# Optimization experiments

Hardware: AMD Instinct MI355X
Metric: run time of the kernel (lower is better)

The kernel has to match this reference:

```python
import jax, jax.numpy as jnp
import numpy as np

D_MODEL = 1024
D_FF = 4096
N_EXPERTS = 8
TOP_K = 2
AUX_COEF = 0.01
ZLOSS_COEF = 0.001
EPS = 1e-9


def setup_inputs() -> dict:
    key = jax.random.key(0)
    k0, k1, k2, k3 = jax.random.split(key, 4)
    x = jax.random.normal(k0, (4, 2048, D_MODEL), dtype=jnp.float32)
    router_w = jax.random.normal(k1, (N_EXPERTS, D_MODEL), dtype=jnp.float32) * 0.02
    w1 = jax.random.normal(k2, (N_EXPERTS, D_FF, D_MODEL), dtype=jnp.float32) * 0.02
    b1 = jnp.zeros((N_EXPERTS, D_FF), dtype=jnp.float32)
    w2 = jax.random.normal(k3, (N_EXPERTS, D_MODEL, D_FF), dtype=jnp.float32) * 0.02
    b2 = jnp.zeros((N_EXPERTS, D_MODEL), dtype=jnp.float32)
    return {"x": x, "router_w": router_w, "w1": w1, "b1": b1, "w2": w2, "b2": b2}


def reference(x, router_w, w1, b1, w2, b2):
    B, T, D = x.shape
    N = B * T
    xf = x.reshape(N, D)

    # Router: logits [N, E], softmax probs, top-k selection + renormalized weights
    logits = jnp.einsum('nd,ed->ne', xf, router_w)
    probs = jax.nn.softmax(logits, axis=-1)
    topk_vals, topk_idx = jax.lax.top_k(probs, TOP_K)  # [N, K]
    topk_w = topk_vals / (topk_vals.sum(axis=-1, keepdims=True) + EPS)

    # Dense combine weights [N, E] (top-k indices are unique per row)
    combine = jnp.zeros((N, N_EXPERTS), dtype=xf.dtype)
    combine = combine.at[jnp.arange(N)[:, None], topk_idx].add(topk_w)

    # Per-expert MLP (fixed small loop over experts), weighted combine.
    # drop_tokens=False => no capacity truncation; masked-dense == gather/scatter math.
    y = jnp.zeros_like(xf)
    for e in range(N_EXPERTS):
        h = jax.nn.gelu(jnp.einsum('nd,fd->nf', xf, w1[e]) + b1[e], approximate=False)
        out_e = jnp.einsum('nf,df->nd', h, w2[e]) + b2[e]
        y = y + out_e * combine[:, e:e + 1]

    # Aux losses / stats
    importance = probs.sum(axis=0)                                   # [E]
    expert_load = jnp.zeros((N_EXPERTS,), jnp.float32).at[topk_idx.reshape(-1)].add(1.0)
    imp_n = importance / (importance.sum() + EPS)
    load_n = expert_load / (expert_load.sum() + EPS)
    balance_loss = N_EXPERTS * jnp.sum(imp_n * load_n)
    z_loss = jnp.mean(jax.nn.logsumexp(logits, axis=-1) ** 2)
    aux_loss = AUX_COEF * balance_loss + ZLOSS_COEF * z_loss

    return y.reshape(B, T, D), aux_loss, expert_load, importance
```

## Files before the change

### kernel.cpp

```cpp
#include <hip/hip_runtime.h>
#include <math.h>

#define NTOK 8192
#define DMODEL 1024
#define DFF 4096
#define NEXP 8
#define TILE 256
#define MAXTILES 72
#define MAXROWS (MAXTILES * TILE)
#define MOE_EPS 1e-9f
#define REG 8192

typedef unsigned short u16;
typedef __bf16 bf16x8 __attribute__((ext_vector_type(8)));
typedef float f32x4 __attribute__((ext_vector_type(4)));

struct Ctrl {
    int counts[NEXP];
    int fill[NEXP];
    int padded_off[NEXP];
    int n_tiles;
    int tile_expert[MAXTILES];
    int tile_base[MAXTILES];
    int tile_valid[MAXTILES];
    float imp[NEXP];
    float zacc;
};

__device__ __forceinline__ u16 f2bf(float f) {
    unsigned u = __float_as_uint(f);
    unsigned r = u + 0x7fffu + ((u >> 16) & 1u);
    return (u16)(r >> 16);
}

__device__ __forceinline__ void load16(const void* g, void* l) {
    __builtin_amdgcn_global_load_lds((__attribute__((address_space(1))) void*)g,
                                     (__attribute__((address_space(3))) void*)l,
                                     16, 0, 0);
}

__device__ __forceinline__ float gelu_fast(float h) {
    float u = h * (1.5957691216f + 0.0713548162f * h * h);
    return h / (1.f + __expf(-u));
}

__global__ __launch_bounds__(256) void k_convert(const float* __restrict__ src,
                                                 u16* __restrict__ dst, int n4) {
    int i = blockIdx.x * 256 + threadIdx.x;
    int stride = gridDim.x * 256;
    for (; i < n4; i += stride) {
        float4 v = ((const float4*)src)[i];
        ushort4 o;
        o.x = f2bf(v.x); o.y = f2bf(v.y); o.z = f2bf(v.z); o.w = f2bf(v.w);
        ((ushort4*)dst)[i] = o;
    }
}

__global__ __launch_bounds__(256) void k_router(const float* __restrict__ x,
                                                const float* __restrict__ rw,
                                                u16* __restrict__ xb,
                                                int* __restrict__ top_idx,
                                                float* __restrict__ top_w,
                                                Ctrl* __restrict__ ctrl) {
    __shared__ float srw[NEXP * DMODEL];
    __shared__ float simp[NEXP];
    __shared__ float szl;
    int tid = threadIdx.x;
    for (int i = tid; i < NEXP * DMODEL / 4; i += 256)
        ((float4*)srw)[i] = ((const float4*)rw)[i];
    if (tid < NEXP) simp[tid] = 0.f;
    if (tid == 0) szl = 0.f;
    __syncthreads();

    int lane = tid & 63;
    int n = blockIdx.x * 4 + (tid >> 6);
    float p[NEXP];
#pragma unroll
    for (int e = 0; e < NEXP; ++e) p[e] = 0.f;
    const float4* xr = (const float4*)(x + (size_t)n * DMODEL);
    u16 xs[16];
#pragma unroll
    for (int j = 0; j < 4; ++j) {
        float4 xv = xr[lane * 4 + j];
        int d = (lane * 4 + j) * 4;
        xs[j * 4 + 0] = f2bf(xv.x);
        xs[j * 4 + 1] = f2bf(xv.y);
        xs[j * 4 + 2] = f2bf(xv.z);
        xs[j * 4 + 3] = f2bf(xv.w);
#pragma unroll
        for (int e = 0; e < NEXP; ++e) {
            const float* r = srw + e * DMODEL + d;
            p[e] += xv.x * r[0] + xv.y * r[1] + xv.z * r[2] + xv.w * r[3];
        }
    }
    {
        uint4* dst = (uint4*)(xb + (size_t)n * DMODEL + lane * 16);
        dst[0] = ((const uint4*)xs)[0];
        dst[1] = ((const uint4*)xs)[1];
    }
#pragma unroll
    for (int e = 0; e < NEXP; ++e) {
#pragma unroll
        for (int off = 32; off > 0; off >>= 1) p[e] += __shfl_xor(p[e], off);
    }
    if (lane == 0) {
        float m = p[0];
#pragma unroll
        for (int e = 1; e < NEXP; ++e) m = fmaxf(m, p[e]);
        float pr[NEXP];
        float s = 0.f;
#pragma unroll
        for (int e = 0; e < NEXP; ++e) { pr[e] = expf(p[e] - m); s += pr[e]; }
        float inv = 1.f / s;
#pragma unroll
        for (int e = 0; e < NEXP; ++e) pr[e] *= inv;
        float lse = m + logf(s);
        int i0 = 0; float v0 = pr[0];
#pragma unroll
        for (int e = 1; e < NEXP; ++e) if (pr[e] > v0) { v0 = pr[e]; i0 = e; }
        int i1 = -1; float v1 = -1.f;
#pragma unroll
        for (int e = 0; e < NEXP; ++e) if (e != i0 && pr[e] > v1) { v1 = pr[e]; i1 = e; }
        float den = v0 + v1 + MOE_EPS;
        top_idx[n * 2] = i0;
        top_idx[n * 2 + 1] = i1;
        top_w[n * 2] = v0 / den;
        top_w[n * 2 + 1] = v1 / den;
#pragma unroll
        for (int e = 0; e < NEXP; ++e) atomicAdd(&simp[e], pr[e]);
        atomicAdd(&szl, lse * lse);
    }
    __syncthreads();
    if (tid < NEXP) atomicAdd(&ctrl->imp[tid], simp[tid]);
    if (tid == 255) atomicAdd(&ctrl->zacc, szl);
}

__global__ __launch_bounds__(256) void k_build(const int* __restrict__ top_idx,
                                               Ctrl* __restrict__ ctrl,
                                               int* __restrict__ tok_idx,
                                               float* __restrict__ tok_w) {
    __shared__ int cnt[NEXP];
    __shared__ int off[NEXP];
    __shared__ int tiles[NEXP];
    int tid = threadIdx.x;
    if (tid < NEXP) cnt[tid] = 0;
    __syncthreads();
    for (int i = tid; i < NTOK * 2; i += 256) atomicAdd(&cnt[top_idx[i]], 1);
    __syncthreads();
    if (tid == 0) {
        int o = 0, t = 0;
        for (int e = 0; e < NEXP; ++e) {
            int c = cnt[e];
            int te = (c + TILE - 1) / TILE;
            ctrl->counts[e] = c;
            ctrl->padded_off[e] = o;
            off[e] = o;
            tiles[e] = te;
            for (int i = 0; i < te; ++i) {
                ctrl->tile_expert[t] = e;
                ctrl->tile_base[t] = o + i * TILE;
                int v = c - i * TILE;
                ctrl->tile_valid[t] = v > TILE ? TILE : v;
                ++t;
            }
            o += te * TILE;
        }
        ctrl->n_tiles = t;
    }
    __syncthreads();
    for (int e = 0; e < NEXP; ++e) {
        int start = off[e] + cnt[e];
        int end = off[e] + tiles[e] * TILE;
        for (int i = start + tid; i < end; i += 256) {
            tok_idx[i] = 0;
            tok_w[i] = 0.f;
        }
    }
}

__global__ __launch_bounds__(256) void k_fill(const int* __restrict__ top_idx,
                                              const float* __restrict__ top_w,
                                              Ctrl* __restrict__ ctrl,
                                              int* __restrict__ tok_idx,
                                              float* __restrict__ tok_w) {
    int n = blockIdx.x * 256 + threadIdx.x;
    if (n >= NTOK) return;
#pragma unroll
    for (int k = 0; k < 2; ++k) {
        int e = top_idx[n * 2 + k];
        int pos = atomicAdd(&ctrl->fill[e], 1);
        int slot = ctrl->padded_off[e] + pos;
        tok_idx[slot] = n;
        tok_w[slot] = top_w[n * 2 + k];
    }
}


#define KLOOP_PHASES(STA, STB, NK)                                                    \
    STA(0, 0, 0); STB(0, 0, 0); STA(0, 0, 1); STB(0, 0, 1); STA(1, 1, 0); STB(1, 1, 0); \
    asm volatile("s_waitcnt vmcnt(8)" ::: "memory");                                  \
    __builtin_amdgcn_s_barrier();                                                     \
    for (int kt = 0; kt < (NK); ++kt) {                                               \
        int p = kt & 1;                                                               \
        const u16* A0 = sA + (p * 2 + 0) * REG;                                       \
        const u16* A1 = sA + (p * 2 + 1) * REG;                                       \
        const u16* B0 = sB + (p * 2 + 0) * REG;                                       \
        const u16* B1 = sB + (p * 2 + 1) * REG;                                       \
        bf16x8 a[4], b[4];                                                            \
                                                    \
        _Pragma("unroll") for (int m = 0; m < 4; ++m) a[m] = *(const bf16x8*)(A0 + aoff[m]); \
        _Pragma("unroll") for (int n = 0; n < 4; ++n) b[n] = *(const bf16x8*)(B0 + boff[n]); \
        if (kt + 1 < (NK)) { STA(p ^ 1, kt + 1, 1); }                                 \
        asm volatile("s_waitcnt lgkmcnt(0)" ::: "memory");                            \
        __builtin_amdgcn_sched_barrier(0);                                            \
        __builtin_amdgcn_s_setprio(1);                                                \
        _Pragma("unroll") for (int m = 0; m < 4; ++m)                                 \
            _Pragma("unroll") for (int n = 0; n < 4; ++n)                             \
                acc[m][n] = __builtin_amdgcn_mfma_f32_16x16x32_bf16(a[m], b[n], acc[m][n], 0, 0, 0); \
        __builtin_amdgcn_s_setprio(0);                                                \
        __builtin_amdgcn_sched_barrier(0);                                            \
        __builtin_amdgcn_s_barrier();                                                 \
                                                    \
        _Pragma("unroll") for (int m = 0; m < 4; ++m) a[m] = *(const bf16x8*)(A0 + aoff[m + 4]); \
        if (kt + 1 < (NK)) { STB(p ^ 1, kt + 1, 1); }                                 \
        asm volatile("s_waitcnt lgkmcnt(0)" ::: "memory");                            \
        __builtin_amdgcn_sched_barrier(0);                                            \
        __builtin_amdgcn_s_setprio(1);                                                \
        _Pragma("unroll") for (int m = 0; m < 4; ++m)                                 \
            _Pragma("unroll") for (int n = 0; n < 4; ++n)                             \
                acc[m + 4][n] = __builtin_amdgcn_mfma_f32_16x16x32_bf16(a[m], b[n], acc[m + 4][n], 0, 0, 0); \
        __builtin_amdgcn_s_setprio(0);                                                \
        __builtin_amdgcn_sched_barrier(0);                                            \
        if (kt <= (NK) - 2) asm volatile("s_waitcnt vmcnt(8)" ::: "memory");          \
        else                asm volatile("s_waitcnt vmcnt(0)" ::: "memory");          \
        __builtin_amdgcn_s_barrier();                                                 \
                                                    \
        _Pragma("unroll") for (int m = 0; m < 4; ++m) a[m] = *(const bf16x8*)(A1 + aoff[m]); \
        _Pragma("unroll") for (int n = 0; n < 4; ++n) b[n] = *(const bf16x8*)(B1 + boff[n]); \
        if (kt + 2 < (NK)) { STA(p, kt + 2, 0); }                                     \
        asm volatile("s_waitcnt lgkmcnt(0)" ::: "memory");                            \
        __builtin_amdgcn_sched_barrier(0);                                            \
        __builtin_amdgcn_s_setprio(1);                                                \
        _Pragma("unroll") for (int m = 0; m < 4; ++m)                                 \
            _Pragma("unroll") for (int n = 0; n < 4; ++n)                             \
                acc[m][n] = __builtin_amdgcn_mfma_f32_16x16x32_bf16(a[m], b[n], acc[m][n], 0, 0, 0); \
        __builtin_amdgcn_s_setprio(0);                                                \
        __builtin_amdgcn_sched_barrier(0);                                            \
        __builtin_amdgcn_s_barrier();                                                 \
                                                    \
        _Pragma("unroll") for (int m = 0; m < 4; ++m) a[m] = *(const bf16x8*)(A1 + aoff[m + 4]); \
        if (kt + 2 < (NK)) { STB(p, kt + 2, 0); }                                     \
        asm volatile("s_waitcnt lgkmcnt(0)" ::: "memory");                            \
        __builtin_amdgcn_sched_barrier(0);                                            \
        __builtin_amdgcn_s_setprio(1);                                                \
        _Pragma("unroll") for (int m = 0; m < 4; ++m)                                 \
            _Pragma("unroll") for (int n = 0; n < 4; ++n)                             \
                acc[m + 4][n] = __builtin_amdgcn_mfma_f32_16x16x32_bf16(a[m], b[n], acc[m + 4][n], 0, 0, 0); \
        __builtin_amdgcn_s_setprio(0);                                                \
        __builtin_amdgcn_sched_barrier(0);                                            \
        if (kt < (NK) - 1) {                                                          \
            if (kt <= (NK) - 3) asm volatile("s_waitcnt vmcnt(8)" ::: "memory");      \
            else                asm volatile("s_waitcnt vmcnt(0)" ::: "memory");      \
            __builtin_amdgcn_s_barrier();                                             \
        }                                                                             \
    }

__global__ __launch_bounds__(512, 2) void k_gemm1(const u16* __restrict__ xb,
                                                  const u16* __restrict__ w1b,
                                                  const float* __restrict__ b1,
                                                  const int* __restrict__ tok_idx,
                                                  const Ctrl* __restrict__ ctrl,
                                                  u16* __restrict__ H) {
    int t = blockIdx.x;
    if (t >= ctrl->n_tiles) return;
    int e = ctrl->tile_expert[t];
    int rbase = ctrl->tile_base[t];
    int n0 = blockIdx.y * TILE;

    __shared__ __align__(16) u16 sA[2 * 2 * REG];
    __shared__ __align__(16) u16 sB[2 * 2 * REG];

    int tid = threadIdx.x;
    const u16* aS[2];
    const u16* bS[2];
    int fo[2];
#pragma unroll
    for (int q = 0; q < 2; ++q) {
        int f = q * 512 + tid;
        int row = f >> 2;
        int lc = (f & 3) ^ ((row >> 1) & 3);
        aS[q] = xb + (size_t)tok_idx[rbase + row] * DMODEL + lc * 8;
        bS[q] = w1b + (size_t)e * DFF * DMODEL + (size_t)(n0 + row) * DMODEL + lc * 8;
        fo[q] = f * 8;
    }

#define STA1(pp, kt, h)                                                               \
    do { _Pragma("unroll") for (int q = 0; q < 2; ++q)                                \
        load16(aS[q] + (kt) * 64 + (h) * 32, &sA[((pp) * 2 + (h)) * REG + fo[q]]); } while (0)
#define STB1(pp, kt, h)                                                               \
    do { _Pragma("unroll") for (int q = 0; q < 2; ++q)                                \
        load16(bS[q] + (kt) * 64 + (h) * 32, &sB[((pp) * 2 + (h)) * REG + fo[q]]); } while (0)

    int lane = tid & 63, w = tid >> 6;
    int wr = w >> 2, wc = w & 3;
    int l15 = lane & 15, lg = lane >> 4;
    int csw = (lg ^ ((l15 >> 1) & 3)) * 8;

    int aoff[8], boff[4];
#pragma unroll
    for (int m = 0; m < 8; ++m) aoff[m] = (wr * 128 + m * 16 + l15) * 32 + csw;
#pragma unroll
    for (int n = 0; n < 4; ++n) boff[n] = (wc * 64 + n * 16 + l15) * 32 + csw;

    f32x4 acc[8][4];
#pragma unroll
    for (int m = 0; m < 8; ++m)
#pragma unroll
        for (int n = 0; n < 4; ++n) acc[m][n] = (f32x4){0.f, 0.f, 0.f, 0.f};

    KLOOP_PHASES(STA1, STB1, DMODEL / 64)
#undef STA1
#undef STB1

    float bias[4];
#pragma unroll
    for (int n = 0; n < 4; ++n) bias[n] = b1[e * DFF + n0 + wc * 64 + n * 16 + l15];
#pragma unroll
    for (int m = 0; m < 8; ++m)
#pragma unroll
        for (int n = 0; n < 4; ++n) {
            int gcol = n0 + wc * 64 + n * 16 + l15;
#pragma unroll
            for (int r = 0; r < 4; ++r) {
                int grow = wr * 128 + m * 16 + lg * 4 + r;
                float h = acc[m][n][r] + bias[n];
                H[(size_t)(rbase + grow) * DFF + gcol] = f2bf(gelu_fast(h));
            }
        }
}

__global__ __launch_bounds__(512, 2) void k_gemm2(const u16* __restrict__ H,
                                                  const u16* __restrict__ w2b,
                                                  const float* __restrict__ b2,
                                                  const int* __restrict__ tok_idx,
                                                  const float* __restrict__ tok_w,
                                                  const Ctrl* __restrict__ ctrl,
                                                  float* __restrict__ y) {
    int t = blockIdx.x;
    if (t >= ctrl->n_tiles) return;
    int e = ctrl->tile_expert[t];
    int rbase = ctrl->tile_base[t];
    int valid = ctrl->tile_valid[t];
    int n0 = blockIdx.y * TILE;

    __shared__ __align__(16) u16 sA[2 * 2 * REG];
    __shared__ __align__(16) u16 sB[2 * 2 * REG];

    int tid = threadIdx.x;
    const u16* aS[2];
    const u16* bS[2];
    int fo[2];
#pragma unroll
    for (int q = 0; q < 2; ++q) {
        int f = q * 512 + tid;
        int row = f >> 2;
        int lc = (f & 3) ^ ((row >> 1) & 3);
        aS[q] = H + (size_t)(rbase + row) * DFF + lc * 8;
        bS[q] = w2b + (size_t)e * DMODEL * DFF + (size_t)(n0 + row) * DFF + lc * 8;
        fo[q] = f * 8;
    }

#define STA2(pp, kt, h)                                                               \
    do { _Pragma("unroll") for (int q = 0; q < 2; ++q)                                \
        load16(aS[q] + (kt) * 64 + (h) * 32, &sA[((pp) * 2 + (h)) * REG + fo[q]]); } while (0)
#define STB2(pp, kt, h)                                                               \
    do { _Pragma("unroll") for (int q = 0; q < 2; ++q)                                \
        load16(bS[q] + (kt) * 64 + (h) * 32, &sB[((pp) * 2 + (h)) * REG + fo[q]]); } while (0)

    int lane = tid & 63, w = tid >> 6;
    int wr = w >> 2, wc = w & 3;
    int l15 = lane & 15, lg = lane >> 4;
    int csw = (lg ^ ((l15 >> 1) & 3)) * 8;

    int aoff[8], boff[4];
#pragma unroll
    for (int m = 0; m < 8; ++m) aoff[m] = (wr * 128 + m * 16 + l15) * 32 + csw;
#pragma unroll
    for (int n = 0; n < 4; ++n) boff[n] = (wc * 64 + n * 16 + l15) * 32 + csw;

    f32x4 acc[8][4];
#pragma unroll
    for (int m = 0; m < 8; ++m)
#pragma unroll
        for (int n = 0; n < 4; ++n) acc[m][n] = (f32x4){0.f, 0.f, 0.f, 0.f};

    KLOOP_PHASES(STA2, STB2, DFF / 64)
#undef STA2
#undef STB2

    float bias[4];
#pragma unroll
    for (int n = 0; n < 4; ++n) bias[n] = b2[e * DMODEL + n0 + wc * 64 + n * 16 + l15];
#pragma unroll
    for (int m = 0; m < 8; ++m)
#pragma unroll
        for (int n = 0; n < 4; ++n) {
            int gcol = n0 + wc * 64 + n * 16 + l15;
#pragma unroll
            for (int r = 0; r < 4; ++r) {
                int grow = wr * 128 + m * 16 + lg * 4 + r;
                if (grow < valid) {
                    int slot = rbase + grow;
                    int tok = tok_idx[slot];
                    float wgt = tok_w[slot];
                    unsafeAtomicAdd(&y[(size_t)tok * DMODEL + gcol],
                                    wgt * (acc[m][n][r] + bias[n]));
                }
            }
        }
}

__global__ void k_final(const Ctrl* __restrict__ ctrl, float* __restrict__ out) {
    if (blockIdx.x == 0 && threadIdx.x == 0) {
        float imp[NEXP], ld[NEXP];
        float imps = 0.f, loads = 0.f;
        for (int e = 0; e < NEXP; ++e) {
            imp[e] = ctrl->imp[e];
            ld[e] = (float)ctrl->counts[e];
            imps += imp[e];
            loads += ld[e];
        }
        float bal = 0.f;
        for (int e = 0; e < NEXP; ++e)
            bal += (imp[e] / (imps + MOE_EPS)) * (ld[e] / (loads + MOE_EPS));
        bal *= (float)NEXP;
        float z = ctrl->zacc / (float)NTOK;
        float aux = 0.01f * bal + 0.001f * z;
        size_t base = (size_t)NTOK * DMODEL;
        out[base] = aux;
        for (int e = 0; e < NEXP; ++e) out[base + 1 + e] = ld[e];
        for (int e = 0; e < NEXP; ++e) out[base + 9 + e] = imp[e];
    }
}

extern "C" void kernel_launch(void* const* d_in, const int* in_sizes, int n_in,
                              void* d_out, int out_size, void* d_ws, size_t ws_size,
                              hipStream_t stream) {
    (void)in_sizes; (void)n_in; (void)out_size; (void)ws_size;
    const float* x  = (const float*)d_in[0];
    const float* rw = (const float*)d_in[1];
    const float* w1 = (const float*)d_in[2];
    const float* b1 = (const float*)d_in[3];
    const float* w2 = (const float*)d_in[4];
    const float* b2 = (const float*)d_in[5];
    float* out = (float*)d_out;

    char* p = (char*)d_ws;
    Ctrl* ctrl = (Ctrl*)p;          p += 4096;
    u16* xb    = (u16*)p;           p += (size_t)NTOK * DMODEL * 2;
    u16* w1b   = (u16*)p;           p += (size_t)NEXP * DFF * DMODEL * 2;
    u16* w2b   = (u16*)p;           p += (size_t)NEXP * DMODEL * DFF * 2;
    u16* Hbuf  = (u16*)p;           p += (size_t)MAXROWS * DFF * 2;
    int* tok_idx = (int*)p;         p += (size_t)MAXROWS * 4;
    float* tok_w = (float*)p;       p += (size_t)MAXROWS * 4;
    int* tIdx  = (int*)p;           p += (size_t)NTOK * 2 * 4;
    float* tW  = (float*)p;         p += (size_t)NTOK * 2 * 4;

    hipMemsetAsync(ctrl, 0, sizeof(Ctrl), stream);
    hipMemsetAsync(d_out, 0, (size_t)NTOK * DMODEL * sizeof(float), stream);

    k_convert<<<2048, 256, 0, stream>>>(w1, w1b, NEXP * DFF * DMODEL / 4);
    k_convert<<<2048, 256, 0, stream>>>(w2, w2b, NEXP * DMODEL * DFF / 4);

    k_router<<<NTOK / 4, 256, 0, stream>>>(x, rw, xb, tIdx, tW, ctrl);
    k_build<<<1, 256, 0, stream>>>(tIdx, ctrl, tok_idx, tok_w);
    k_fill<<<NTOK / 256, 256, 0, stream>>>(tIdx, tW, ctrl, tok_idx, tok_w);

    dim3 g1(MAXTILES, DFF / TILE);
    k_gemm1<<<g1, 512, 0, stream>>>(xb, w1b, b1, tok_idx, ctrl, Hbuf);

    dim3 g2(MAXTILES, DMODEL / TILE);
    k_gemm2<<<g2, 512, 0, stream>>>(Hbuf, w2b, b2, tok_idx, tok_w, ctrl, out);

    k_final<<<1, 64, 0, stream>>>(ctrl, out);
}
```

Before: 841.9 us.

## Restructure GEMM k-loop pipeline, swizzle tile order, split-K second GEMM

The shared k-loop macro is reworked so global-to-LDS loads are issued in a different order with a vmcnt(6) wait before each phase, giving deeper prefetch. Both GEMMs switch to a flat 1D grid whose index is remapped so groups of eight row tiles share a column tile, which is meant to improve L2 reuse of weights. The second GEMM is split along K into two halves that both atomically add into the output, doubling its block count to improve occupancy. Launch bounds drop to one block per CU, which gives more registers but may lower latency hiding.

```diff
diff --git a/kernel.cpp b/kernel.cpp
--- a/kernel.cpp
+++ b/kernel.cpp
@@ -195,11 +195,9 @@
     }
 }
 
-
-#define KLOOP_PHASES(STA, STB, NK)                                                    \
-    STA(0, 0, 0); STB(0, 0, 0); STA(0, 0, 1); STB(0, 0, 1); STA(1, 1, 0); STB(1, 1, 0); \
-    asm volatile("s_waitcnt vmcnt(8)" ::: "memory");                                  \
-    __builtin_amdgcn_s_barrier();                                                     \
+#define KLOOP8(SA, SB, NK)                                                            \
+    SA(0, 0, 0); SB(0, 0, 0); SA(0, 0, 1); SB(0, 0, 1);                               \
+    SB(1, 1, 0); SA(1, 1, 0); SB(1, 1, 1);                                            \
     for (int kt = 0; kt < (NK); ++kt) {                                               \
         int p = kt & 1;                                                               \
         const u16* A0 = sA + (p * 2 + 0) * REG;                                       \
@@ -207,10 +205,14 @@
         const u16* B0 = sB + (p * 2 + 0) * REG;                                       \
         const u16* B1 = sB + (p * 2 + 1) * REG;                                       \
         bf16x8 a[4], b[4];                                                            \
-                                                    \
+        int last = (kt == (NK) - 1);                                                  \
+                                                                   \
+        if (last) asm volatile("s_waitcnt vmcnt(0)" ::: "memory");                    \
+        else      asm volatile("s_waitcnt vmcnt(6)" ::: "memory");                    \
+        __builtin_amdgcn_s_barrier();                                                 \
         _Pragma("unroll") for (int m = 0; m < 4; ++m) a[m] = *(const bf16x8*)(A0 + aoff[m]); \
         _Pragma("unroll") for (int n = 0; n < 4; ++n) b[n] = *(const bf16x8*)(B0 + boff[n]); \
-        if (kt + 1 < (NK)) { STA(p ^ 1, kt + 1, 1); }                                 \
+        if (kt + 1 < (NK)) { SA(p ^ 1, kt + 1, 1); }                                  \
         asm volatile("s_waitcnt lgkmcnt(0)" ::: "memory");                            \
         __builtin_amdgcn_sched_barrier(0);                                            \
         __builtin_amdgcn_s_setprio(1);                                                \
@@ -219,10 +221,12 @@
                 acc[m][n] = __builtin_amdgcn_mfma_f32_16x16x32_bf16(a[m], b[n], acc[m][n], 0, 0, 0); \
         __builtin_amdgcn_s_setprio(0);                                                \
         __builtin_amdgcn_sched_barrier(0);                                            \
+                                                                   \
+        if (last) asm volatile("s_waitcnt vmcnt(0)" ::: "memory");                    \
+        else      asm volatile("s_waitcnt vmcnt(6)" ::: "memory");                    \
         __builtin_amdgcn_s_barrier();                                                 \
-                                                    \
         _Pragma("unroll") for (int m = 0; m < 4; ++m) a[m] = *(const bf16x8*)(A0 + aoff[m + 4]); \
-        if (kt + 1 < (NK)) { STB(p ^ 1, kt + 1, 1); }                                 \
+        if (kt + 2 < (NK)) { SB(p, kt + 2, 0); }                                      \
         asm volatile("s_waitcnt lgkmcnt(0)" ::: "memory");                            \
         __builtin_amdgcn_sched_barrier(0);                                            \
         __builtin_amdgcn_s_setprio(1);                                                \
@@ -231,13 +235,13 @@
                 acc[m + 4][n] = __builtin_amdgcn_mfma_f32_16x16x32_bf16(a[m], b[n], acc[m + 4][n], 0, 0, 0); \
         __builtin_amdgcn_s_setprio(0);                                                \
         __builtin_amdgcn_sched_barrier(0);                                            \
-        if (kt <= (NK) - 2) asm volatile("s_waitcnt vmcnt(8)" ::: "memory");          \
-        else                asm volatile("s_waitcnt vmcnt(0)" ::: "memory");          \
+                                                                   \
+        if (last) asm volatile("s_waitcnt vmcnt(0)" ::: "memory");                    \
+        else      asm volatile("s_waitcnt vmcnt(6)" ::: "memory");                    \
         __builtin_amdgcn_s_barrier();                                                 \
-                                                    \
         _Pragma("unroll") for (int m = 0; m < 4; ++m) a[m] = *(const bf16x8*)(A1 + aoff[m]); \
         _Pragma("unroll") for (int n = 0; n < 4; ++n) b[n] = *(const bf16x8*)(B1 + boff[n]); \
-        if (kt + 2 < (NK)) { STA(p, kt + 2, 0); }                                     \
+        if (kt + 2 < (NK)) { SA(p, kt + 2, 0); }                                      \
         asm volatile("s_waitcnt lgkmcnt(0)" ::: "memory");                            \
         __builtin_amdgcn_sched_barrier(0);                                            \
         __builtin_amdgcn_s_setprio(1);                                                \
@@ -246,10 +250,12 @@
                 acc[m][n] = __builtin_amdgcn_mfma_f32_16x16x32_bf16(a[m], b[n], acc[m][n], 0, 0, 0); \
         __builtin_amdgcn_s_setprio(0);                                                \
         __builtin_amdgcn_sched_barrier(0);                                            \
+                                                                   \
+        if (last) asm volatile("s_waitcnt vmcnt(0)" ::: "memory");                    \
+        else      asm volatile("s_waitcnt vmcnt(6)" ::: "memory");                    \
         __builtin_amdgcn_s_barrier();                                                 \
-                                                    \
         _Pragma("unroll") for (int m = 0; m < 4; ++m) a[m] = *(const bf16x8*)(A1 + aoff[m + 4]); \
-        if (kt + 2 < (NK)) { STB(p, kt + 2, 0); }                                     \
+        if (kt + 2 < (NK)) { SB(p, kt + 2, 1); }                                      \
         asm volatile("s_waitcnt lgkmcnt(0)" ::: "memory");                            \
         __builtin_amdgcn_sched_barrier(0);                                            \
         __builtin_amdgcn_s_setprio(1);                                                \
@@ -258,24 +264,20 @@
                 acc[m + 4][n] = __builtin_amdgcn_mfma_f32_16x16x32_bf16(a[m], b[n], acc[m + 4][n], 0, 0, 0); \
         __builtin_amdgcn_s_setprio(0);                                                \
         __builtin_amdgcn_sched_barrier(0);                                            \
-        if (kt < (NK) - 1) {                                                          \
-            if (kt <= (NK) - 3) asm volatile("s_waitcnt vmcnt(8)" ::: "memory");      \
-            else                asm volatile("s_waitcnt vmcnt(0)" ::: "memory");      \
-            __builtin_amdgcn_s_barrier();                                             \
-        }                                                                             \
-    }
-
-__global__ __launch_bounds__(512, 2) void k_gemm1(const u16* __restrict__ xb,
+    }
+
+__global__ __launch_bounds__(512, 1) void k_gemm1(const u16* __restrict__ xb,
                                                   const u16* __restrict__ w1b,
                                                   const float* __restrict__ b1,
                                                   const int* __restrict__ tok_idx,
                                                   const Ctrl* __restrict__ ctrl,
                                                   u16* __restrict__ H) {
-    int t = blockIdx.x;
+    int flat = blockIdx.x;
+    int t = (flat & 7) + ((flat >> 7) << 3);
+    int n0 = ((flat >> 3) & 15) * TILE;
     if (t >= ctrl->n_tiles) return;
     int e = ctrl->tile_expert[t];
     int rbase = ctrl->tile_base[t];
-    int n0 = blockIdx.y * TILE;
 
     __shared__ __align__(16) u16 sA[2 * 2 * REG];
     __shared__ __align__(16) u16 sB[2 * 2 * REG];
@@ -294,12 +296,12 @@
         fo[q] = f * 8;
     }
 
-#define STA1(pp, kt, h)                                                               \
+#define SA1(pp, kt, kk)                                                               \
     do { _Pragma("unroll") for (int q = 0; q < 2; ++q)                                \
-        load16(aS[q] + (kt) * 64 + (h) * 32, &sA[((pp) * 2 + (h)) * REG + fo[q]]); } while (0)
-#define STB1(pp, kt, h)                                                               \
+        load16(aS[q] + (kt) * 64 + (kk) * 32, &sA[((pp) * 2 + (kk)) * REG + fo[q]]); } while (0)
+#define SB1(pp, kt, kk)                                                               \
     do { _Pragma("unroll") for (int q = 0; q < 2; ++q)                                \
-        load16(bS[q] + (kt) * 64 + (h) * 32, &sB[((pp) * 2 + (h)) * REG + fo[q]]); } while (0)
+        load16(bS[q] + (kt) * 64 + (kk) * 32, &sB[((pp) * 2 + (kk)) * REG + fo[q]]); } while (0)
 
     int lane = tid & 63, w = tid >> 6;
     int wr = w >> 2, wc = w & 3;
@@ -318,9 +320,9 @@
 #pragma unroll
         for (int n = 0; n < 4; ++n) acc[m][n] = (f32x4){0.f, 0.f, 0.f, 0.f};
 
-    KLOOP_PHASES(STA1, STB1, DMODEL / 64)
-#undef STA1
-#undef STB1
+    KLOOP8(SA1, SB1, DMODEL / 64)
+#undef SA1
+#undef SB1
 
     float bias[4];
 #pragma unroll
@@ -339,19 +341,22 @@
         }
 }
 
-__global__ __launch_bounds__(512, 2) void k_gemm2(const u16* __restrict__ H,
+__global__ __launch_bounds__(512, 1) void k_gemm2(const u16* __restrict__ H,
                                                   const u16* __restrict__ w2b,
                                                   const float* __restrict__ b2,
                                                   const int* __restrict__ tok_idx,
                                                   const float* __restrict__ tok_w,
                                                   const Ctrl* __restrict__ ctrl,
                                                   float* __restrict__ y) {
-    int t = blockIdx.x;
+    int flat = blockIdx.x;
+    int t = (flat & 7) + ((flat >> 6) << 3);
+    int n0 = ((flat >> 3) & 3) * TILE;
+    int chunk = (flat >> 5) & 1;
     if (t >= ctrl->n_tiles) return;
     int e = ctrl->tile_expert[t];
     int rbase = ctrl->tile_base[t];
     int valid = ctrl->tile_valid[t];
-    int n0 = blockIdx.y * TILE;
+    int kbase = chunk * (DFF / 2);
 
     __shared__ __align__(16) u16 sA[2 * 2 * REG];
     __shared__ __align__(16) u16 sB[2 * 2 * REG];
@@ -365,17 +370,17 @@
         int f = q * 512 + tid;
         int row = f >> 2;
         int lc = (f & 3) ^ ((row >> 1) & 3);
-        aS[q] = H + (size_t)(rbase + row) * DFF + lc * 8;
-        bS[q] = w2b + (size_t)e * DMODEL * DFF + (size_t)(n0 + row) * DFF + lc * 8;
+        aS[q] = H + (size_t)(rbase + row) * DFF + kbase + lc * 8;
+        bS[q] = w2b + (size_t)e * DMODEL * DFF + (size_t)(n0 + row) * DFF + kbase + lc * 8;
         fo[q] = f * 8;
     }
 
-#define STA2(pp, kt, h)                                                               \
+#define SA2(pp, kt, kk)                                                               \
     do { _Pragma("unroll") for (int q = 0; q < 2; ++q)                                \
-        load16(aS[q] + (kt) * 64 + (h) * 32, &sA[((pp) * 2 + (h)) * REG + fo[q]]); } while (0)
-#define STB2(pp, kt, h)                                                               \
+        load16(aS[q] + (kt) * 64 + (kk) * 32, &sA[((pp) * 2 + (kk)) * REG + fo[q]]); } while (0)
+#define SB2(pp, kt, kk)                                                               \
     do { _Pragma("unroll") for (int q = 0; q < 2; ++q)                                \
-        load16(bS[q] + (kt) * 64 + (h) * 32, &sB[((pp) * 2 + (h)) * REG + fo[q]]); } while (0)
+        load16(bS[q] + (kt) * 64 + (kk) * 32, &sB[((pp) * 2 + (kk)) * REG + fo[q]]); } while (0)
 
     int lane = tid & 63, w = tid >> 6;
     int wr = w >> 2, wc = w & 3;
@@ -394,13 +399,14 @@
 #pragma unroll
         for (int n = 0; n < 4; ++n) acc[m][n] = (f32x4){0.f, 0.f, 0.f, 0.f};
 
-    KLOOP_PHASES(STA2, STB2, DFF / 64)
-#undef STA2
-#undef STB2
+    KLOOP8(SA2, SB2, DFF / 64 / 2)
+#undef SA2
+#undef SB2
 
     float bias[4];
 #pragma unroll
-    for (int n = 0; n < 4; ++n) bias[n] = b2[e * DMODEL + n0 + wc * 64 + n * 16 + l15];
+    for (int n = 0; n < 4; ++n)
+        bias[n] = (chunk == 0) ? b2[e * DMODEL + n0 + wc * 64 + n * 16 + l15] : 0.f;
 #pragma unroll
     for (int m = 0; m < 8; ++m)
 #pragma unroll
@@ -476,11 +482,8 @@
     k_build<<<1, 256, 0, stream>>>(tIdx, ctrl, tok_idx, tok_w);
     k_fill<<<NTOK / 256, 256, 0, stream>>>(tIdx, tW, ctrl, tok_idx, tok_w);
 
-    dim3 g1(MAXTILES, DFF / TILE);
-    k_gemm1<<<g1, 512, 0, stream>>>(xb, w1b, b1, tok_idx, ctrl, Hbuf);
-
-    dim3 g2(MAXTILES, DMODEL / TILE);
-    k_gemm2<<<g2, 512, 0, stream>>>(Hbuf, w2b, b2, tok_idx, tok_w, ctrl, out);
+    k_gemm1<<<MAXTILES * (DFF / TILE), 512, 0, stream>>>(xb, w1b, b1, tok_idx, ctrl, Hbuf);
+    k_gemm2<<<MAXTILES * (DMODEL / TILE) * 2, 512, 0, stream>>>(Hbuf, w2b, b2, tok_idx, tok_w, ctrl, out);
 
     k_final<<<1, 64, 0, stream>>>(ctrl, out);
 }
```

Result: slower. 874.4 us (+3.9%).
